# Kernel tuning notes

Measured on AMD Instinct MI355X. Metric: run time of the kernel, lower is better.

The kernel has to match this reference:

```python
import jax, jax.numpy as jnp
import numpy as np

B, T, E, H = 4, 2048, 1024, 16
D = E // H
PAD_TOKEN_ID = 0
VOCAB = 50257


def setup_inputs() -> dict:
    key = jax.random.key(0)
    k1, k2, k3, k4 = jax.random.split(key, 4)
    x = jax.random.normal(k1, (B, T, E), dtype=jnp.float32)
    input_ids = jax.random.randint(k2, (B, T), 0, VOCAB, dtype=jnp.int64)
    # guarantee first key of every sequence is non-pad so no softmax row is fully masked
    input_ids = input_ids.at[:, 0].set(1)
    w_qkv = jax.random.normal(k3, (E, 3 * E), dtype=jnp.float32) * 0.02
    w_out = jax.random.normal(k4, (E, E), dtype=jnp.float32) * 0.02
    b_out = jnp.zeros((E,), dtype=jnp.float32)
    return {"x": x, "input_ids": input_ids, "w_qkv": w_qkv, "w_out": w_out, "b_out": b_out}


def reference(x, input_ids, w_qkv, w_out, b_out):
    b, t, e = x.shape
    # fused QKV projection (bias=False in original)
    qkv = x @ w_qkv                                   # [B,T,3E]
    q, k, v = jnp.split(qkv, 3, axis=-1)
    q = q.reshape(b, t, H, D).transpose(0, 2, 1, 3)   # [B,H,T,D]
    k = k.reshape(b, t, H, D).transpose(0, 2, 1, 3)
    v = v.reshape(b, t, H, D).transpose(0, 2, 1, 3)

    scale = 1.0 / jnp.sqrt(jnp.asarray(D, dtype=x.dtype))
    scores = jnp.einsum("bhqd,bhkd->bhqk", q, k) * scale   # [B,H,T,T]

    causal = jnp.tril(jnp.ones((t, t), dtype=bool))         # [T,T]
    key_keep = (input_ids != PAD_TOKEN_ID)[:, None, None, :]  # [B,1,1,T]
    mask = causal[None, None, :, :] & key_keep               # [B,1(T broadcast over H),T,T]
    scores = jnp.where(mask, scores, -jnp.inf)

    attn = jax.nn.softmax(scores, axis=-1)                   # dropout_p=0 in eval
    y = jnp.einsum("bhqk,bhkd->bhqd", attn, v)               # [B,H,T,D]
    y = y.transpose(0, 2, 1, 3).reshape(b, t, e)             # [B,T,E]
    return y @ w_out + b_out
```

## Files before the change

kernel.cpp:

```cpp
#include <hip/hip_runtime.h>
#include <hip/hip_bf16.h>
#include <stdint.h>

#define Hn 16
#define Tn 2048
#define En 1024
#define Dh 64

typedef __bf16 bf16x8 __attribute__((ext_vector_type(8)));
typedef float f32x4 __attribute__((ext_vector_type(4)));
typedef unsigned short u16;
typedef u16 u16x8 __attribute__((ext_vector_type(8)));

#define SCALE_Q 0.18033688f

__device__ __forceinline__ u16 f2bf(float f) {
  __bf16 b = (__bf16)f;
  return __builtin_bit_cast(u16, b);
}

typedef const __attribute__((address_space(1))) void gvoid_t;
typedef __attribute__((address_space(3))) void lvoid_t;
__device__ __forceinline__ void gl_lds16(const void* g, void* l) {
  __builtin_amdgcn_global_load_lds((gvoid_t*)g, (lvoid_t*)l, 16, 0, 0);
}

__global__ void cvt_x_k(const float* __restrict__ in, u16* __restrict__ out) {
  int i = (blockIdx.x * 256 + threadIdx.x) * 8;
  float4 a = *(const float4*)(in + i);
  float4 b = *(const float4*)(in + i + 4);
  u16x8 o;
  o[0] = f2bf(a.x); o[1] = f2bf(a.y); o[2] = f2bf(a.z); o[3] = f2bf(a.w);
  o[4] = f2bf(b.x); o[5] = f2bf(b.y); o[6] = f2bf(b.z); o[7] = f2bf(b.w);
  *(u16x8*)(out + i) = o;
}

__global__ void transpose_cvt_k(const float* __restrict__ in, u16* __restrict__ out,
                                int R, int C) {
  __shared__ float tile[32][33];
  int c0 = blockIdx.x * 32, r0 = blockIdx.y * 32;
  for (int i = threadIdx.y; i < 32; i += 8)
    tile[i][threadIdx.x] = in[(size_t)(r0 + i) * C + c0 + threadIdx.x];
  __syncthreads();
  for (int i = threadIdx.y; i < 32; i += 8)
    out[(size_t)(c0 + i) * R + r0 + threadIdx.x] = f2bf(tile[threadIdx.x][i]);
}

__global__ void prep_mask_k(const int* __restrict__ in, u16* __restrict__ maskh) {
  __shared__ int is64_s;
  if (threadIdx.x == 0) {
    int all0 = 1;
    for (int i = 1; i < 256; i += 2) all0 &= (in[i] == 0);
    is64_s = all0;
  }
  __syncthreads();
  int i = blockIdx.x * 256 + threadIdx.x;
  int v = is64_s ? in[2 * i] : in[i];
  maskh[i] = (v != 0) ? (u16)0 : f2bf(-1e30f);
}

__device__ __forceinline__ void gemm_mainloop(const u16* __restrict__ A,
                                              const u16* __restrict__ Bt,
                                              int K, int m0, int n0,
                                              u16* lds, f32x4 acc[4][4]) {
  const int tid = threadIdx.x;
  const int lane = tid & 63;
  const int w = tid >> 6;
  const int wm = (w >> 1) * 64, wn = (w & 1) * 64;
  const int quad = lane >> 4, ln = lane & 15;

  const int e0 = w * 512 + lane * 8;
  const int r0 = e0 >> 6;
  const int cS = (e0 & 63) ^ ((r0 & 7) * 8);

  const u16* gA = A + (size_t)(m0 + r0) * K + cS;
  const u16* gB = Bt + (size_t)(n0 + r0) * K + cS;
  u16* lA = lds + e0;
  u16* lB = lds + 8192 + e0;
  const int xA = (ln & 7) * 8;

  for (int k0 = 0; k0 < K; k0 += 64) {
#pragma unroll
    for (int c = 0; c < 4; c++) {
      gl_lds16(gA + (size_t)(c * 32) * K + k0, lA + c * 2048);
      gl_lds16(gB + (size_t)(c * 32) * K + k0, lB + c * 2048);
    }
    __syncthreads();
#pragma unroll
    for (int kk = 0; kk < 2; kk++) {
      bf16x8 af[4], bfr[4];
#pragma unroll
      for (int mt = 0; mt < 4; mt++)
        af[mt] = *(const bf16x8*)(lds + (wm + mt * 16 + ln) * 64 +
                                  ((kk * 32 + quad * 8) ^ xA));
#pragma unroll
      for (int nt = 0; nt < 4; nt++)
        bfr[nt] = *(const bf16x8*)(lds + 8192 + (wn + nt * 16 + ln) * 64 +
                                   ((kk * 32 + quad * 8) ^ xA));
#pragma unroll
      for (int mt = 0; mt < 4; mt++)
#pragma unroll
        for (int nt = 0; nt < 4; nt++)
          acc[mt][nt] = __builtin_amdgcn_mfma_f32_16x16x32_bf16(af[mt], bfr[nt],
                                                                acc[mt][nt], 0, 0, 0);
    }
    __syncthreads();
  }
}

__global__ __launch_bounds__(256, 3)
void gemm_qkv_kernel(const u16* __restrict__ X, const u16* __restrict__ Wt,
                     u16* __restrict__ Qo, u16* __restrict__ Ko,
                     u16* __restrict__ Vto) {
  __shared__ __align__(16) u16 lds[128 * 130];
  const int m0 = blockIdx.y * 128, n0 = blockIdx.x * 128;
  f32x4 acc[4][4];
#pragma unroll
  for (int i = 0; i < 4; i++)
#pragma unroll
    for (int j = 0; j < 4; j++) acc[i][j] = (f32x4){0.f, 0.f, 0.f, 0.f};

  gemm_mainloop(X, Wt, En, m0, n0, lds, acc);

  const int tid = threadIdx.x, lane = tid & 63, w = tid >> 6;
  const int wm = (w >> 1) * 64, wn = (w & 1) * 64;
  const int quad = lane >> 4, ln = lane & 15;
  const int which = n0 >> 10;
  const int bb = m0 >> 11, t0 = m0 & (Tn - 1);

  if (which < 2) {
#pragma unroll
    for (int mt = 0; mt < 4; mt++)
#pragma unroll
      for (int nt = 0; nt < 4; nt++)
#pragma unroll
        for (int r = 0; r < 4; r++) {
          int t = t0 + wm + mt * 16 + quad * 4 + r;
          int ng = n0 + wn + nt * 16 + ln;
          int e = ng & (En - 1);
          int h = e >> 6, d = e & 63;
          size_t bh = (size_t)(bb * Hn + h);
          if (which == 0)
            Qo[(bh * Tn + t) * Dh + d] = f2bf(acc[mt][nt][r] * SCALE_Q);
          else
            Ko[(bh * Tn + t) * Dh + d] = f2bf(acc[mt][nt][r]);
        }
  } else {
#pragma unroll
    for (int mt = 0; mt < 4; mt++)
#pragma unroll
      for (int nt = 0; nt < 4; nt++)
#pragma unroll
        for (int r = 0; r < 4; r++)
          lds[(wm + mt * 16 + quad * 4 + r) * 130 + wn + nt * 16 + ln] =
              f2bf(acc[mt][nt][r]);
    __syncthreads();
    const int ebase = n0 & (En - 1);
#pragma unroll
    for (int i = 0; i < 32; i++) {
      int col = w * 32 + i;
      int e = ebase + col;
      int hh = e >> 6, d = e & 63;
      size_t vrow = (((size_t)(bb * Hn + hh)) * Dh + d) * Tn + t0;
      Vto[vrow + lane] = lds[lane * 130 + col];
      Vto[vrow + 64 + lane] = lds[(64 + lane) * 130 + col];
    }
  }
}

__global__ __launch_bounds__(256, 3)
void gemm_out_kernel(const u16* __restrict__ Y, const u16* __restrict__ Wt,
                     const float* __restrict__ bias, float* __restrict__ Out) {
  __shared__ __align__(16) u16 lds[16384];
  const int m0 = blockIdx.y * 128, n0 = blockIdx.x * 128;
  f32x4 acc[4][4];
#pragma unroll
  for (int i = 0; i < 4; i++)
#pragma unroll
    for (int j = 0; j < 4; j++) acc[i][j] = (f32x4){0.f, 0.f, 0.f, 0.f};

  gemm_mainloop(Y, Wt, En, m0, n0, lds, acc);

  const int tid = threadIdx.x, lane = tid & 63, w = tid >> 6;
  const int wm = (w >> 1) * 64, wn = (w & 1) * 64;
  const int quad = lane >> 4, ln = lane & 15;

#pragma unroll
  for (int mt = 0; mt < 4; mt++)
#pragma unroll
    for (int nt = 0; nt < 4; nt++)
#pragma unroll
      for (int r = 0; r < 4; r++) {
        int mg = m0 + wm + mt * 16 + quad * 4 + r;
        int ng = n0 + wn + nt * 16 + ln;
        Out[(size_t)mg * En + ng] = acc[mt][nt][r] + bias[ng];
      }
}

__global__ __launch_bounds__(256, 3)
void attn_kernel(const u16* __restrict__ Q, const u16* __restrict__ K,
                 const u16* __restrict__ Vt, const u16* __restrict__ maskh,
                 u16* __restrict__ Y) {
  __shared__ __align__(16) u16 Pl[128 * 76];
  __shared__ __align__(16) u16 KL[2 * 4096];
  __shared__ __align__(16) u16 ML[2048];

  const int bid = blockIdx.x;
  const int g = bid >> 8, sq = (bid >> 6) & 3;
  int qt;
  if (g == 0)      qt = 15 - sq;
  else if (g == 1) qt = sq;
  else if (g == 2) qt = 11 - sq;
  else             qt = 4 + sq;
  const int bh = bid & 63;
  const int b = bh >> 4, h = bh & 15;
  const int tid = threadIdx.x, lane = tid & 63, w = tid >> 6;
  const int quad = lane >> 4, ln = lane & 15;
  const int qb = w * 32;
  const int g0 = qt * 128 + qb;

  const size_t baseQK = (size_t)bh * (Tn * Dh);
  const size_t baseV = (size_t)bh * (Dh * Tn);
  const u16* Kp = K + baseQK;

  const int srow = tid >> 3;
  const int scol = ((tid & 7) * 8) ^ ((srow & 7) * 8);
  const u16* gK0 = Kp + (size_t)srow * Dh + scol;
  const u16* gK1 = Kp + (size_t)(srow + 32) * Dh + scol;
  u16* lK0 = KL + tid * 8;
  u16* lK1 = lK0 + 2048;

  auto stage = [&](int buf, int k0) {
    gl_lds16(gK0 + (size_t)k0 * Dh, lK0 + buf * 4096);
    gl_lds16(gK1 + (size_t)k0 * Dh, lK1 + buf * 4096);
  };

  gl_lds16(maskh + (size_t)b * Tn + tid * 8, ML + tid * 8);

  bf16x8 aq[2][2];
#pragma unroll
  for (int rt = 0; rt < 2; rt++)
#pragma unroll
    for (int ks = 0; ks < 2; ks++)
      aq[rt][ks] = *(const bf16x8*)(Q + baseQK +
          (size_t)(g0 + rt * 16 + ln) * Dh + ks * 32 + quad * 8);

  bf16x8 onesb;
#pragma unroll
  for (int i = 0; i < 8; i++) onesb[i] = (__bf16)1.0f;

  f32x4 O[2][4];
  f32x4 ls[2];
#pragma unroll
  for (int rt = 0; rt < 2; rt++) {
#pragma unroll
    for (int dt = 0; dt < 4; dt++) O[rt][dt] = (f32x4){0.f, 0.f, 0.f, 0.f};
    ls[rt] = (f32x4){0.f, 0.f, 0.f, 0.f};
  }

  auto tile = [&](const u16* kl, int k0, bool dg) {
    f32x4 s[2][4];
    {
      bf16x8 bk[4][2];
      float kvf[4];
#pragma unroll
      for (int ct = 0; ct < 4; ct++) {
        kvf[ct] = __builtin_bit_cast(float,
                      (uint32_t)ML[k0 + ct * 16 + ln] << 16);
#pragma unroll
        for (int ks = 0; ks < 2; ks++)
          bk[ct][ks] = *(const bf16x8*)(kl + (ct * 16 + ln) * 64 +
                                        ((ks * 32 + quad * 8) ^ ((ln & 7) * 8)));
      }
#pragma unroll
      for (int rt = 0; rt < 2; rt++)
#pragma unroll
        for (int ct = 0; ct < 4; ct++)
          s[rt][ct] = (f32x4){kvf[ct], kvf[ct], kvf[ct], kvf[ct]};
      __builtin_amdgcn_s_setprio(1);
#pragma unroll
      for (int ks = 0; ks < 2; ks++)
#pragma unroll
        for (int rt = 0; rt < 2; rt++)
#pragma unroll
          for (int ct = 0; ct < 4; ct++)
            s[rt][ct] = __builtin_amdgcn_mfma_f32_16x16x32_bf16(aq[rt][ks], bk[ct][ks],
                                                                s[rt][ct], 0, 0, 0);
      __builtin_amdgcn_s_setprio(0);
    }

    bf16x8 bv[4][2];
#pragma unroll
    for (int dt = 0; dt < 4; dt++)
#pragma unroll
      for (int ks = 0; ks < 2; ks++)
        bv[dt][ks] = *(const bf16x8*)(Vt + baseV +
            (size_t)(dt * 16 + ln) * Tn + k0 + ks * 32 + quad * 8);

#pragma unroll
    for (int rt = 0; rt < 2; rt++) {
      if (dg) {
#pragma unroll
        for (int ct = 0; ct < 4; ct++)
#pragma unroll
          for (int r = 0; r < 4; r++) {
            int qg = g0 + rt * 16 + quad * 4 + r;
            int kg = k0 + ct * 16 + ln;
            float v = (kg > qg) ? -1e30f : s[rt][ct][r];
            float p = exp2f(fminf(v, 126.f));
            Pl[(qb + rt * 16 + quad * 4 + r) * 76 + ct * 16 + ln] = f2bf(p);
          }
      } else {
#pragma unroll
        for (int ct = 0; ct < 4; ct++)
#pragma unroll
          for (int r = 0; r < 4; r++) {
            float p = exp2f(fminf(s[rt][ct][r], 126.f));
            Pl[(qb + rt * 16 + quad * 4 + r) * 76 + ct * 16 + ln] = f2bf(p);
          }
      }
    }

    __builtin_amdgcn_s_setprio(1);
#pragma unroll
    for (int ks2 = 0; ks2 < 2; ks2++)
#pragma unroll
      for (int rt = 0; rt < 2; rt++) {
        bf16x8 ap = *(const bf16x8*)(Pl + (qb + rt * 16 + ln) * 76 + ks2 * 32 + quad * 8);
#pragma unroll
        for (int dt = 0; dt < 4; dt++)
          O[rt][dt] = __builtin_amdgcn_mfma_f32_16x16x32_bf16(ap, bv[dt][ks2],
                                                              O[rt][dt], 0, 0, 0);
        ls[rt] = __builtin_amdgcn_mfma_f32_16x16x32_bf16(ap, onesb,
                                                         ls[rt], 0, 0, 0);
      }
    __builtin_amdgcn_s_setprio(0);
  };

  const int nfull = g0 >> 6;
  const int NT = 2 * qt + 1;
  stage(0, 0);
  int cur = 0;
  for (int kt = 0; kt <= NT; kt++) {
    __syncthreads();
    if (kt < NT) stage(cur ^ 1, (kt + 1) * 64);
    if (kt < nfull)       tile(KL + cur * 4096, kt * 64, false);
    else if (kt == nfull) tile(KL + cur * 4096, kt * 64, true);
    cur ^= 1;
  }

#pragma unroll
  for (int rt = 0; rt < 2; rt++)
#pragma unroll
    for (int r = 0; r < 4; r++) {
      float inv = 1.f / ls[rt][r];
      int tg = g0 + rt * 16 + quad * 4 + r;
      size_t ob = ((size_t)b * Tn + tg) * En + h * Dh;
#pragma unroll
      for (int dt = 0; dt < 4; dt++)
        Y[ob + dt * 16 + ln] = f2bf(O[rt][dt][r] * inv);
    }
}

#define OFF_MASK  0
#define OFF_WQKVT 16384
#define OFF_WOUTT (OFF_WQKVT + 3145728)
#define OFF_Q     (OFF_WOUTT + 1048576)
#define OFF_K     (OFF_Q + 8388608)
#define OFF_XY    (OFF_K + 8388608)

extern "C" void kernel_launch(void* const* d_in, const int* in_sizes, int n_in,
                              void* d_out, int out_size, void* d_ws, size_t ws_size,
                              hipStream_t stream) {
  const float* x = nullptr;
  const int* ids_raw = nullptr;
  const float* wqkv = nullptr;
  const float* wout = nullptr;
  const float* bias = nullptr;
  for (int i = 0; i < n_in; i++) {
    switch (in_sizes[i]) {
      case 8388608: x = (const float*)d_in[i]; break;
      case 8192:    ids_raw = (const int*)d_in[i]; break;
      case 3145728: wqkv = (const float*)d_in[i]; break;
      case 1048576: wout = (const float*)d_in[i]; break;
      case 1024:    bias = (const float*)d_in[i]; break;
      default: break;
    }
  }
  if (!x) x = (const float*)d_in[0];
  if (!ids_raw) ids_raw = (const int*)d_in[1];
  if (!wqkv) wqkv = (const float*)d_in[2];
  if (!wout) wout = (const float*)d_in[3];
  if (!bias) bias = (const float*)d_in[4];

  u16* ws = (u16*)d_ws;
  u16* maskh = ws + OFF_MASK;
  u16* wqkv_t = ws + OFF_WQKVT;
  u16* wout_t = ws + OFF_WOUTT;
  u16* Qb = ws + OFF_Q;
  u16* Kb = ws + OFF_K;
  u16* XbYb = ws + OFF_XY;
  u16* Vtb = (u16*)d_out;
  float* out = (float*)d_out;

  prep_mask_k<<<32, 256, 0, stream>>>(ids_raw, maskh);
  cvt_x_k<<<4096, 256, 0, stream>>>(x, XbYb);
  transpose_cvt_k<<<dim3(96, 32), dim3(32, 8), 0, stream>>>(wqkv, wqkv_t, 1024, 3072);
  transpose_cvt_k<<<dim3(32, 32), dim3(32, 8), 0, stream>>>(wout, wout_t, 1024, 1024);
  gemm_qkv_kernel<<<dim3(24, 64), 256, 0, stream>>>(XbYb, wqkv_t, Qb, Kb, Vtb);
  attn_kernel<<<1024, 256, 0, stream>>>(Qb, Kb, Vtb, maskh, XbYb);
  gemm_out_kernel<<<dim3(8, 64), 256, 0, stream>>>(XbYb, wout_t, bias, out);
}
```

Baseline: 283.5 us.

## Double-buffer GEMM mainloop with K-step 32 and prefetch next tile

Changes the shared GEMM mainloop from a single-buffered K=64 tile to two LDS buffers of K=32 each. The next tile is loaded asynchronously while MFMAs run on the current one. This overlaps global-to-LDS loads with compute, uses one barrier per iteration instead of two, and keeps total LDS use the same. The cost is twice as many loop iterations with less compute per barrier, and the XOR swizzle is rewritten for the new 32-wide row layout.

Result: no change. 284.1 us (+0.2%).

```diff
diff --git a/kernel.cpp b/kernel.cpp
--- a/kernel.cpp
+++ b/kernel.cpp
@@ -70,42 +70,44 @@
   const int quad = lane >> 4, ln = lane & 15;
 
   const int e0 = w * 512 + lane * 8;
-  const int r0 = e0 >> 6;
-  const int cS = (e0 & 63) ^ ((r0 & 7) * 8);
+  const int r0 = e0 >> 5;
+  const int cS = (e0 & 31) ^ (((r0 >> 1) & 3) * 8);
 
   const u16* gA = A + (size_t)(m0 + r0) * K + cS;
   const u16* gB = Bt + (size_t)(n0 + r0) * K + cS;
-  u16* lA = lds + e0;
-  u16* lB = lds + 8192 + e0;
-  const int xA = (ln & 7) * 8;
-
-  for (int k0 = 0; k0 < K; k0 += 64) {
-#pragma unroll
-    for (int c = 0; c < 4; c++) {
-      gl_lds16(gA + (size_t)(c * 32) * K + k0, lA + c * 2048);
-      gl_lds16(gB + (size_t)(c * 32) * K + k0, lB + c * 2048);
-    }
+  const int xR = ((ln >> 1) & 3) * 8;
+
+  auto stage = [&](int buf, int k0) {
+    u16* lA = lds + buf * 8192 + e0;
+    u16* lB = lA + 4096;
+    gl_lds16(gA + k0, lA);
+    gl_lds16(gA + (size_t)64 * K + k0, lA + 2048);
+    gl_lds16(gB + k0, lB);
+    gl_lds16(gB + (size_t)64 * K + k0, lB + 2048);
+  };
+
+  stage(0, 0);
+  int cur = 0;
+  for (int k0 = 0; k0 < K; k0 += 32) {
     __syncthreads();
-#pragma unroll
-    for (int kk = 0; kk < 2; kk++) {
-      bf16x8 af[4], bfr[4];
-#pragma unroll
-      for (int mt = 0; mt < 4; mt++)
-        af[mt] = *(const bf16x8*)(lds + (wm + mt * 16 + ln) * 64 +
-                                  ((kk * 32 + quad * 8) ^ xA));
+    if (k0 + 32 < K) stage(cur ^ 1, k0 + 32);
+    const u16* lb = lds + cur * 8192;
+    bf16x8 af[4], bfr[4];
+#pragma unroll
+    for (int mt = 0; mt < 4; mt++)
+      af[mt] = *(const bf16x8*)(lb + (wm + mt * 16 + ln) * 32 + ((quad * 8) ^ xR));
+#pragma unroll
+    for (int nt = 0; nt < 4; nt++)
+      bfr[nt] = *(const bf16x8*)(lb + 4096 + (wn + nt * 16 + ln) * 32 + ((quad * 8) ^ xR));
+#pragma unroll
+    for (int mt = 0; mt < 4; mt++)
 #pragma unroll
       for (int nt = 0; nt < 4; nt++)
-        bfr[nt] = *(const bf16x8*)(lds + 8192 + (wn + nt * 16 + ln) * 64 +
-                                   ((kk * 32 + quad * 8) ^ xA));
-#pragma unroll
-      for (int mt = 0; mt < 4; mt++)
-#pragma unroll
-        for (int nt = 0; nt < 4; nt++)
-          acc[mt][nt] = __builtin_amdgcn_mfma_f32_16x16x32_bf16(af[mt], bfr[nt],
-                                                                acc[mt][nt], 0, 0, 0);
-    }
-    __syncthreads();
-  }
+        acc[mt][nt] = __builtin_amdgcn_mfma_f32_16x16x32_bf16(af[mt], bfr[nt],
+                                                              acc[mt][nt], 0, 0, 0);
+    cur ^= 1;
+  }
+  __syncthreads();
 }
 
 __global__ __launch_bounds__(256, 3)
```
